# Kernel tuning notes

Hardware: AMD Instinct MI355X
Metric: run time of the kernel (lower is better)

The kernel has to match this reference:

```python
import jax, jax.numpy as jnp
import numpy as np

B, C_IN, C_OUT, T, K, STRIDE, PAD = 16, 256, 256, 4096, 3, 1, 1


def deform_conv1d(x, offset, weight, bias):
    # x: (B,C,T); offset: (B,2K,Tout,1) interleaved (dy,dx); weight: (O,C,K); bias: (O,)
    Bn, C, Tn = x.shape
    O, _, Kn = weight.shape
    dy = offset[:, 0::2, :, 0]  # (B,K,Tout)
    dx = offset[:, 1::2, :, 0]  # (B,K,Tout)
    Tout = dy.shape[-1]
    # offset_mode='center': subtract dcn_base_offset (y base = k-pad, x base = 0)
    base_y = jnp.arange(Kn, dtype=x.dtype) - PAD
    dy = dy - base_y[None, :, None]
    # sampling position along T: t*stride - pad + k + dy
    t0 = jnp.arange(Tout, dtype=x.dtype) * STRIDE - PAD
    py = t0[None, None, :] + jnp.arange(Kn, dtype=x.dtype)[None, :, None] + dy  # (B,K,Tout)
    i0 = jnp.floor(py)
    frac = py - i0
    i0i = i0.astype(jnp.int32)

    def gather(idx):
        valid = ((idx >= 0) & (idx < Tn)).astype(x.dtype)  # zero padding outside
        idxc = jnp.clip(idx, 0, Tn - 1).reshape(Bn, 1, Kn * Tout)
        v = jnp.take_along_axis(x, jnp.broadcast_to(idxc, (Bn, C, Kn * Tout)), axis=2)
        return v.reshape(Bn, C, Kn, Tout) * valid[:, None]

    # linear interp along T
    v = gather(i0i) * (1.0 - frac)[:, None] + gather(i0i + 1) * frac[:, None]  # (B,C,K,Tout)
    # bilinear weight along the dummy width dim (W=1, base x index 0)
    wx = jnp.maximum(0.0, 1.0 - jnp.abs(dx))  # (B,K,Tout)
    v = v * wx[:, None]
    out = jnp.einsum('bckt,ock->bot', v, weight) + bias[None, :, None]
    return out


def setup_inputs() -> dict:
    key = jax.random.key(0)
    k1, k2, k3, k4 = jax.random.split(key, 4)
    x = jax.random.normal(k1, (B, C_IN, T), dtype=jnp.float32)
    offset = jax.random.normal(k2, (B, 2 * K, T, 1), dtype=jnp.float32)
    fan_in = C_IN * K
    bound = 1.0 / np.sqrt(fan_in)
    weight = jax.random.uniform(k3, (C_OUT, C_IN, K), minval=-bound, maxval=bound, dtype=jnp.float32)
    bias = jax.random.uniform(k4, (C_OUT,), minval=-bound, maxval=bound, dtype=jnp.float32)
    return {"x": x, "offset": offset, "weight": weight, "bias": bias}


def reference(x, offset, weight, bias):
    return deform_conv1d(x, offset, weight, bias)
```

## Files before the change

kernel.cpp:

```cpp
#include <hip/hip_runtime.h>
#include <hip/hip_bf16.h>

typedef __attribute__((ext_vector_type(8))) short bf16x8;
typedef __attribute__((ext_vector_type(4))) float f32x4;

constexpr int NB = 16, CIN = 256, COUT = 256, TDIM = 4096, KS = 3, PADV = 1;
constexpr int TT = 64;
constexpr int NSTEP = 12;

typedef __attribute__((address_space(1))) const unsigned int gu32;
typedef __attribute__((address_space(3))) unsigned int lu32;

static __device__ __forceinline__ ushort f2bf(float f) {
    union { __hip_bfloat16 h; ushort u; } cv;
    cv.h = __float2bfloat16(f);
    return cv.u;
}
static __device__ __forceinline__ float bf2f(ushort u) {
    union { unsigned int u32; float f; } cv;
    cv.u32 = ((unsigned int)u) << 16;
    return cv.f;
}

__global__ __launch_bounds__(256) void prepack_w2(const float* __restrict__ w,
                                                  __hip_bfloat16* __restrict__ wp2) {
    int idx = blockIdx.x * 256 + threadIdx.x;
    if (idx >= NSTEP * COUT * 64) return;
    int e    = idx & 7;
    int lane = (idx >> 3) & 63;
    int mf   = (idx >> 9) & 1;
    int kb   = (idx >> 10) & 1;
    int wid  = (idx >> 11) & 3;
    int ot   = (idx >> 13) & 1;
    int s    = idx >> 14;
    int o = ot * 128 + wid * 32 + mf * 16 + (lane & 15);
    int k = s % 3;
    int c = (s / 3) * 64 + kb * 32 + (lane >> 4) * 8 + e;
    wp2[idx] = __float2bfloat16(w[(o * CIN + c) * KS + k]);
}

__global__ __launch_bounds__(256) void prepack_w(const float* __restrict__ w,
                                                 __hip_bfloat16* __restrict__ wp) {
    int idx = blockIdx.x * 256 + threadIdx.x;
    if (idx >= NSTEP * COUT * 64) return;
    int e  = idx & 7;
    int j  = (idx >> 3) & 7;
    int o  = (idx >> 6) & (COUT - 1);
    int s  = idx >> 14;
    int k  = s % 3;
    int c  = (s / 3) * 64 + ((j ^ (o & 7)) << 3) + e;
    wp[idx] = __float2bfloat16(w[(o * CIN + c) * KS + k]);
}

__global__ __launch_bounds__(256) void transpose_x(const float* __restrict__ x,
                                                   ushort* __restrict__ xT) {
    __shared__ ushort tile[64][72];
    const int b  = blockIdx.z;
    const int c0 = blockIdx.y * 64;
    const int t0 = blockIdx.x * 64;
    const int tid = threadIdx.x;
    {
        const int c  = tid >> 2;
        const int tq = (tid & 3) << 4;
        const float* src = x + ((size_t)(b * CIN + c0 + c)) * TDIM + t0 + tq;
        #pragma unroll
        for (int i = 0; i < 4; ++i) {
            float4 f = *(const float4*)(src + 4 * i);
            tile[tq + 4 * i + 0][c] = f2bf(f.x);
            tile[tq + 4 * i + 1][c] = f2bf(f.y);
            tile[tq + 4 * i + 2][c] = f2bf(f.z);
            tile[tq + 4 * i + 3][c] = f2bf(f.w);
        }
    }
    __syncthreads();
    {
        const int t = tid >> 2;
        const int q = tid & 3;
        const uint4* lp = (const uint4*)&tile[t][q * 16];
        uint4 v0 = lp[0], v1 = lp[1];
        uint4* dst = (uint4*)(xT + ((size_t)b * TDIM + t0 + t) * CIN + c0 + q * 16);
        dst[0] = v0;
        dst[1] = v1;
    }
}

__global__ __launch_bounds__(256, 4) void deform_mfma_xt(
    const ushort* __restrict__ xT,
    const float* __restrict__ off,
    const ushort* __restrict__ wp2,
    const float* __restrict__ bias,
    float* __restrict__ out)
{
    __shared__ ushort v_s[TT * 64];
    __shared__ int4   sP[KS][TT];

    const int tid = threadIdx.x;

    const int bid = blockIdx.x;
    const int q   = bid & 7;
    const int r   = bid >> 3;
    const int b   = 2 * q + (r >> 7);
    const int r2  = r & 127;
    const int ot  = r2 >> 6;
    const int tt0 = (r2 & 63) * TT;

    if (tid < KS * TT) {
        int k = tid >> 6, j = tid & (TT - 1);
        int t = tt0 + j;
        float dyr = off[((b * 2 * KS + 2 * k) * TDIM) + t];
        float dxr = off[((b * 2 * KS + 2 * k + 1) * TDIM) + t];
        float dyk = dyr - (float)(k - PADV);
        float py  = (float)(t - PADV + k) + dyk;
        float i0f = floorf(py);
        float fr  = py - i0f;
        int i0 = (int)i0f, i1 = i0 + 1;
        float wx = fmaxf(0.0f, 1.0f - fabsf(dxr));
        float w0 = (1.0f - fr) * wx * ((i0 >= 0 && i0 < TDIM) ? 1.0f : 0.0f);
        float w1 = fr * wx * ((i1 >= 0 && i1 < TDIM) ? 1.0f : 0.0f);
        int base = min(max(i0, 0), TDIM - 2);
        bool iA = (i0 == base);
        float wa = iA ? w0 : ((i0 + 1 == base) ? w1 : 0.0f);
        float wb = iA ? w1 : ((i0 == base + 1) ? w0 : 0.0f);
        int4 p;
        p.x = base;
        p.y = __float_as_int(wa);
        p.z = __float_as_int(wb);
        p.w = 0;
        sP[k][j] = p;
    }

    const int wid  = tid >> 6;
    const int lane = tid & 63;
    const int lr   = lane & 15;
    const int lg   = lane >> 4;

    const int tg   = tid >> 3;
    const int slot = tid & 7;
    const int t0l  = tg;
    const int t1l  = tg + 32;
    const int voffA = (t0l * 128 + slot * 16) ^ ((t0l & 7) << 4);
    const int voffB = (t1l * 128 + slot * 16) ^ ((t1l & 7) << 4);

    f32x4 acc[2][4];
    #pragma unroll
    for (int i = 0; i < 2; ++i)
        #pragma unroll
        for (int j = 0; j < 4; ++j) acc[i][j] = (f32x4)0.0f;

    const ushort* xTb = xT + (size_t)b * TDIM * CIN;

    __syncthreads();

    bf16x8 af0, af1, af2, af3;
    bf16x8 pk0, pk1;
    {
        const ushort* wslot = wp2 + (size_t)(((0 * 2 + ot) * 4 + wid) * 4) * 512 + lane * 8;
        af0 = *(const bf16x8*)(wslot);
        af1 = *(const bf16x8*)(wslot + 512);
        af2 = *(const bf16x8*)(wslot + 1024);
        af3 = *(const bf16x8*)(wslot + 1536);
        int4 e0 = sP[0][t0l];
        int4 e1 = sP[0][t1l];
        const ushort* rowA = xTb + (size_t)e0.x * CIN + slot * 8;
        const ushort* rowB = xTb + (size_t)e1.x * CIN + slot * 8;
        bf16x8 a0 = *(const bf16x8*)rowA;
        bf16x8 a1 = *(const bf16x8*)(rowA + CIN);
        bf16x8 b0 = *(const bf16x8*)rowB;
        bf16x8 b1 = *(const bf16x8*)(rowB + CIN);
        float wa0 = __int_as_float(e0.y), wb0 = __int_as_float(e0.z);
        float wa1 = __int_as_float(e1.y), wb1 = __int_as_float(e1.z);
        #pragma unroll
        for (int i = 0; i < 8; ++i) {
            pk0[i] = (short)f2bf(bf2f((ushort)a0[i]) * wa0 + bf2f((ushort)a1[i]) * wb0);
            pk1[i] = (short)f2bf(bf2f((ushort)b0[i]) * wa1 + bf2f((ushort)b1[i]) * wb1);
        }
    }

    #pragma unroll 1
    for (int s = 0; s < NSTEP; ++s) {
        const int sn  = (s + 1 < NSTEP) ? s + 1 : NSTEP - 1;
        const int kn  = sn % 3;
        const int cbn = (sn / 3) * 64;

        __builtin_amdgcn_s_barrier();
        __builtin_amdgcn_sched_barrier(0);

        *(bf16x8*)((char*)v_s + voffA) = pk0;
        *(bf16x8*)((char*)v_s + voffB) = pk1;

        const ushort* wslot = wp2 + (size_t)(((sn * 2 + ot) * 4 + wid) * 4) * 512 + lane * 8;
        bf16x8 an0 = *(const bf16x8*)(wslot);
        bf16x8 an1 = *(const bf16x8*)(wslot + 512);
        bf16x8 an2 = *(const bf16x8*)(wslot + 1024);
        bf16x8 an3 = *(const bf16x8*)(wslot + 1536);

        int4 e0 = sP[kn][t0l];
        int4 e1 = sP[kn][t1l];
        const ushort* rowA = xTb + (size_t)e0.x * CIN + cbn + slot * 8;
        const ushort* rowB = xTb + (size_t)e1.x * CIN + cbn + slot * 8;
        bf16x8 ga0 = *(const bf16x8*)rowA;
        bf16x8 ga1 = *(const bf16x8*)(rowA + CIN);
        bf16x8 gb0 = *(const bf16x8*)rowB;
        bf16x8 gb1 = *(const bf16x8*)(rowB + CIN);

        __builtin_amdgcn_sched_barrier(0);
        asm volatile("s_waitcnt lgkmcnt(0)" ::: "memory");
        __builtin_amdgcn_sched_barrier(0);
        __builtin_amdgcn_s_barrier();
        __builtin_amdgcn_sched_barrier(0);

        #pragma unroll
        for (int kb = 0; kb < 2; ++kb) {
            const int kk = kb * 32 + lg * 8;
            bf16x8 bfr[4];
            #pragma unroll
            for (int nf = 0; nf < 4; ++nf) {
                int tc = nf * 16 + lr;
                int byte = (tc * 128 + kk * 2) ^ ((tc & 7) << 4);
                bfr[nf] = *(const bf16x8*)((const char*)v_s + byte);
            }
            bf16x8 a0 = kb ? af2 : af0;
            bf16x8 a1 = kb ? af3 : af1;
            #pragma unroll
            for (int nf = 0; nf < 4; ++nf) {
                acc[0][nf] = __builtin_amdgcn_mfma_f32_16x16x32_bf16(a0, bfr[nf], acc[0][nf], 0, 0, 0);
                acc[1][nf] = __builtin_amdgcn_mfma_f32_16x16x32_bf16(a1, bfr[nf], acc[1][nf], 0, 0, 0);
            }
        }
        __builtin_amdgcn_sched_barrier(0);

        {
            float wa0 = __int_as_float(e0.y), wb0 = __int_as_float(e0.z);
            float wa1 = __int_as_float(e1.y), wb1 = __int_as_float(e1.z);
            #pragma unroll
            for (int i = 0; i < 8; ++i) {
                pk0[i] = (short)f2bf(bf2f((ushort)ga0[i]) * wa0 + bf2f((ushort)ga1[i]) * wb0);
                pk1[i] = (short)f2bf(bf2f((ushort)gb0[i]) * wa1 + bf2f((ushort)gb1[i]) * wb1);
            }
        }
        af0 = an0; af1 = an1; af2 = an2; af3 = an3;
    }

    #pragma unroll
    for (int mf = 0; mf < 2; ++mf) {
        #pragma unroll
        for (int rg = 0; rg < 4; ++rg) {
            int o = ot * 128 + wid * 32 + mf * 16 + lg * 4 + rg;
            float bv = bias[o];
            float* orow = out + (size_t)(b * COUT + o) * TDIM + tt0;
            #pragma unroll
            for (int nf = 0; nf < 4; ++nf)
                orow[nf * 16 + lr] = acc[mf][nf][rg] + bv;
        }
    }
}

__global__ __launch_bounds__(512, 4) void deform_mfma_gather(
    const float* __restrict__ x,
    const float* __restrict__ off,
    const __hip_bfloat16* __restrict__ wp,
    const float* __restrict__ bias,
    float* __restrict__ out)
{
    __shared__ ushort w_s[COUT * 64];
    __shared__ ushort v_s[128 * 64];
    __shared__ int4   sP[KS][128];

    const int tid = threadIdx.x;
    const int bid  = blockIdx.x;
    const int q    = bid & 7;
    const int r    = bid >> 3;
    const int b    = 2 * q + (r >> 5);
    const int tt0  = (r & 31) * 128;

    if (tid < KS * 128) {
        int k = tid >> 7, j = tid & 127;
        int t = tt0 + j;
        float dyr = off[((b * 2 * KS + 2 * k) * TDIM) + t];
        float dxr = off[((b * 2 * KS + 2 * k + 1) * TDIM) + t];
        float py  = (float)(t - PADV + k) + dyr - (float)(k - PADV);
        float i0f = floorf(py);
        float fr  = py - i0f;
        int i0 = (int)i0f, i1 = i0 + 1;
        float wx = fmaxf(0.0f, 1.0f - fabsf(dxr));
        float w0 = (1.0f - fr) * wx * ((i0 >= 0 && i0 < TDIM) ? 1.0f : 0.0f);
        float w1 = fr * wx * ((i1 >= 0 && i1 < TDIM) ? 1.0f : 0.0f);
        int4 p;
        p.x = min(max(i0, 0), TDIM - 1);
        p.y = min(max(i1, 0), TDIM - 1);
        p.z = __float_as_int(w0);
        p.w = __float_as_int(w1);
        sP[k][j] = p;
    }

    const int wid    = tid >> 6;
    const int lane   = tid & 63;
    const int o_base = (wid >> 1) * 64;
    const int t_base = (wid & 1) * 64;
    const int lr     = lane & 15;
    const int lg     = lane >> 4;

    f32x4 acc[4][4];
    #pragma unroll
    for (int i = 0; i < 4; ++i)
        #pragma unroll
        for (int j = 0; j < 4; ++j) acc[i][j] = (f32x4)0.0f;

    const float* xb = x + (size_t)b * CIN * TDIM;

    for (int cb = 0; cb < 4; ++cb) {
      for (int k = 0; k < 3; ++k) {
        const int s_idx = cb * 3 + k;
        const int c0    = cb * 64;
        __syncthreads();
        {
            const char* gbase = (const char*)wp + (size_t)s_idx * 32768 + wid * 4096 + lane * 16;
            char* lbase = (char*)w_s + wid * 4096;
            #pragma unroll
            for (int i = 0; i < 4; ++i)
                __builtin_amdgcn_global_load_lds((gu32*)(gbase + i * 1024),
                                                 (lu32*)(lbase + i * 1024), 16, 0, 0);
        }
        {
            const int coct0 = tid >> 7;
            const int t     = tid & 127;
            int4 p = sP[k][t];
            const float* xr0 = xb + (size_t)(c0 + coct0 * 8) * TDIM;
            const float* xr1 = xr0 + (size_t)32 * TDIM;
            float g0[16], g1[16];
            #pragma unroll
            for (int i = 0; i < 8; ++i) {
                g0[2 * i]     = xr0[p.x];
                g0[2 * i + 1] = xr0[p.y];
                xr0 += TDIM;
            }
            #pragma unroll
            for (int i = 0; i < 8; ++i) {
                g1[2 * i]     = xr1[p.x];
                g1[2 * i + 1] = xr1[p.y];
                xr1 += TDIM;
            }
            float w0 = __int_as_float(p.z), w1 = __int_as_float(p.w);
            bf16x8 pk0, pk1;
            #pragma unroll
            for (int i = 0; i < 8; ++i) {
                pk0[i] = (short)f2bf(g0[2 * i] * w0 + g0[2 * i + 1] * w1);
                pk1[i] = (short)f2bf(g1[2 * i] * w0 + g1[2 * i + 1] * w1);
            }
            int row = t * 128;
            int swz = (t & 7) << 4;
            *(bf16x8*)((char*)v_s + ((row + coct0 * 16) ^ swz))       = pk0;
            *(bf16x8*)((char*)v_s + ((row + (coct0 + 4) * 16) ^ swz)) = pk1;
        }
        __syncthreads();
        #pragma unroll
        for (int kb = 0; kb < 2; ++kb) {
            const int kk = kb * 32 + lg * 8;
            bf16x8 bfr[4];
            #pragma unroll
            for (int nf = 0; nf < 4; ++nf) {
                int tc = t_base + nf * 16 + lr;
                int byte = (tc * 128 + kk * 2) ^ ((tc & 7) << 4);
                bfr[nf] = *(const bf16x8*)((const char*)v_s + byte);
            }
            #pragma unroll
            for (int mf = 0; mf < 4; ++mf) {
                int o  = o_base + mf * 16 + lr;
                int byte = (o * 128 + kk * 2) ^ ((o & 7) << 4);
                bf16x8 af = *(const bf16x8*)((const char*)w_s + byte);
                #pragma unroll
                for (int nf = 0; nf < 4; ++nf)
                    acc[mf][nf] = __builtin_amdgcn_mfma_f32_16x16x32_bf16(
                        af, bfr[nf], acc[mf][nf], 0, 0, 0);
            }
        }
      }
    }

    #pragma unroll
    for (int mf = 0; mf < 4; ++mf) {
        #pragma unroll
        for (int rg = 0; rg < 4; ++rg) {
            int o = o_base + mf * 16 + lg * 4 + rg;
            float bv = bias[o];
            float* orow = out + (size_t)(b * COUT + o) * TDIM + tt0 + t_base;
            #pragma unroll
            for (int nf = 0; nf < 4; ++nf)
                orow[nf * 16 + lr] = acc[mf][nf][rg] + bv;
        }
    }
}

extern "C" void kernel_launch(void* const* d_in, const int* in_sizes, int n_in,
                              void* d_out, int out_size, void* d_ws, size_t ws_size,
                              hipStream_t stream) {
    const float* x    = (const float*)d_in[0];
    const float* off  = (const float*)d_in[1];
    const float* w    = (const float*)d_in[2];
    const float* bias = (const float*)d_in[3];
    float* out = (float*)d_out;

    const size_t xt_off  = 512 * 1024;
    const size_t xt_need = xt_off + (size_t)NB * TDIM * CIN * sizeof(ushort);

    if (ws_size >= xt_need) {
        ushort* wp2 = (ushort*)d_ws;
        ushort* xT  = (ushort*)((char*)d_ws + xt_off);
        prepack_w2<<<dim3(768), dim3(256), 0, stream>>>(w, (__hip_bfloat16*)wp2);
        transpose_x<<<dim3(TDIM / 64, CIN / 64, NB), dim3(256), 0, stream>>>(x, xT);
        deform_mfma_xt<<<dim3(2048), dim3(256), 0, stream>>>(xT, off, wp2, bias, out);
    } else {
        __hip_bfloat16* wp = (__hip_bfloat16*)d_ws;
        prepack_w<<<dim3(768), dim3(256), 0, stream>>>(w, wp);
        deform_mfma_gather<<<dim3(512), dim3(512), 0, stream>>>(x, off, wp, bias, out);
    }
}
```

Measured before the change: 70.86 us.

## Fuse weight prepack into transpose, use packed bf16 interpolation and nontemporal stores

Merges the weight prepack kernel into the x transpose kernel, removing one launch. The interpolation now runs as packed bf16x2 multiply-adds with weights pre-rounded to bf16 and duplicated into both halves, where it previously unpacked to float. Row offsets are pre-multiplied by CIN, and output stores are marked nontemporal. The bf16 arithmetic lowers interpolation precision, which risks a larger numeric error.

```diff
diff --git a/kernel.cpp b/kernel.cpp
--- a/kernel.cpp
+++ b/kernel.cpp
@@ -3,6 +3,7 @@
 
 typedef __attribute__((ext_vector_type(8))) short bf16x8;
 typedef __attribute__((ext_vector_type(4))) float f32x4;
+typedef __attribute__((ext_vector_type(2))) __bf16 bf16x2v;
 
 constexpr int NB = 16, CIN = 256, COUT = 256, TDIM = 4096, KS = 3, PADV = 1;
 constexpr int TT = 64;
@@ -16,27 +17,72 @@
     cv.h = __float2bfloat16(f);
     return cv.u;
 }
-static __device__ __forceinline__ float bf2f(ushort u) {
-    union { unsigned int u32; float f; } cv;
-    cv.u32 = ((unsigned int)u) << 16;
-    return cv.f;
-}
-
-__global__ __launch_bounds__(256) void prepack_w2(const float* __restrict__ w,
-                                                  __hip_bfloat16* __restrict__ wp2) {
-    int idx = blockIdx.x * 256 + threadIdx.x;
-    if (idx >= NSTEP * COUT * 64) return;
-    int e    = idx & 7;
-    int lane = (idx >> 3) & 63;
-    int mf   = (idx >> 9) & 1;
-    int kb   = (idx >> 10) & 1;
-    int wid  = (idx >> 11) & 3;
-    int ot   = (idx >> 13) & 1;
-    int s    = idx >> 14;
-    int o = ot * 128 + wid * 32 + mf * 16 + (lane & 15);
-    int k = s % 3;
-    int c = (s / 3) * 64 + kb * 32 + (lane >> 4) * 8 + e;
-    wp2[idx] = __float2bfloat16(w[(o * CIN + c) * KS + k]);
+
+static __device__ __forceinline__ bf16x8 interp8_pk(bf16x8 a0, bf16x8 a1,
+                                                    unsigned int waa, unsigned int wbb) {
+    union U { unsigned int u; bf16x2v v; };
+    union { bf16x8 v; unsigned int u[4]; } A0, A1, R;
+    A0.v = a0; A1.v = a1;
+    U wa2; wa2.u = waa;
+    U wb2; wb2.u = wbb;
+    #pragma unroll
+    for (int j = 0; j < 4; ++j) {
+        U p0; p0.u = A0.u[j];
+        U p1; p1.u = A1.u[j];
+        U r;  r.v = p0.v * wa2.v + p1.v * wb2.v;
+        R.u[j] = r.u;
+    }
+    return R.v;
+}
+
+__global__ __launch_bounds__(256) void transpose_prepack(
+    const float* __restrict__ x, ushort* __restrict__ xT,
+    const float* __restrict__ w, __hip_bfloat16* __restrict__ wp2) {
+    __shared__ ushort tile[64][72];
+    const int b  = blockIdx.z;
+    const int c0 = blockIdx.y * 64;
+    const int t0 = blockIdx.x * 64;
+    const int tid = threadIdx.x;
+    {
+        int gid = ((blockIdx.z * gridDim.y + blockIdx.y) * gridDim.x + blockIdx.x);
+        if (tid < 48) {
+            int idx = gid * 48 + tid;
+            int e    = idx & 7;
+            int lane = (idx >> 3) & 63;
+            int mf   = (idx >> 9) & 1;
+            int kb   = (idx >> 10) & 1;
+            int wid  = (idx >> 11) & 3;
+            int ot   = (idx >> 13) & 1;
+            int s    = idx >> 14;
+            int o = ot * 128 + wid * 32 + mf * 16 + (lane & 15);
+            int k = s % 3;
+            int c = (s / 3) * 64 + kb * 32 + (lane >> 4) * 8 + e;
+            wp2[idx] = __float2bfloat16(w[(o * CIN + c) * KS + k]);
+        }
+    }
+    {
+        const int c  = tid >> 2;
+        const int tq = (tid & 3) << 4;
+        const float* src = x + ((size_t)(b * CIN + c0 + c)) * TDIM + t0 + tq;
+        #pragma unroll
+        for (int i = 0; i < 4; ++i) {
+            float4 f = *(const float4*)(src + 4 * i);
+            tile[tq + 4 * i + 0][c] = f2bf(f.x);
+            tile[tq + 4 * i + 1][c] = f2bf(f.y);
+            tile[tq + 4 * i + 2][c] = f2bf(f.z);
+            tile[tq + 4 * i + 3][c] = f2bf(f.w);
+        }
+    }
+    __syncthreads();
+    {
+        const int t = tid >> 2;
+        const int q = tid & 3;
+        const uint4* lp = (const uint4*)&tile[t][q * 16];
+        uint4 v0 = lp[0], v1 = lp[1];
+        uint4* dst = (uint4*)(xT + ((size_t)b * TDIM + t0 + t) * CIN + c0 + q * 16);
+        dst[0] = v0;
+        dst[1] = v1;
+    }
 }
 
 __global__ __launch_bounds__(256) void prepack_w(const float* __restrict__ w,
@@ -50,38 +96,6 @@
     int k  = s % 3;
     int c  = (s / 3) * 64 + ((j ^ (o & 7)) << 3) + e;
     wp[idx] = __float2bfloat16(w[(o * CIN + c) * KS + k]);
-}
-
-__global__ __launch_bounds__(256) void transpose_x(const float* __restrict__ x,
-                                                   ushort* __restrict__ xT) {
-    __shared__ ushort tile[64][72];
-    const int b  = blockIdx.z;
-    const int c0 = blockIdx.y * 64;
-    const int t0 = blockIdx.x * 64;
-    const int tid = threadIdx.x;
-    {
-        const int c  = tid >> 2;
-        const int tq = (tid & 3) << 4;
-        const float* src = x + ((size_t)(b * CIN + c0 + c)) * TDIM + t0 + tq;
-        #pragma unroll
-        for (int i = 0; i < 4; ++i) {
-            float4 f = *(const float4*)(src + 4 * i);
-            tile[tq + 4 * i + 0][c] = f2bf(f.x);
-            tile[tq + 4 * i + 1][c] = f2bf(f.y);
-            tile[tq + 4 * i + 2][c] = f2bf(f.z);
-            tile[tq + 4 * i + 3][c] = f2bf(f.w);
-        }
-    }
-    __syncthreads();
-    {
-        const int t = tid >> 2;
-        const int q = tid & 3;
-        const uint4* lp = (const uint4*)&tile[t][q * 16];
-        uint4 v0 = lp[0], v1 = lp[1];
-        uint4* dst = (uint4*)(xT + ((size_t)b * TDIM + t0 + t) * CIN + c0 + q * 16);
-        dst[0] = v0;
-        dst[1] = v1;
-    }
 }
 
 __global__ __launch_bounds__(256, 4) void deform_mfma_xt(
@@ -121,10 +135,12 @@
         bool iA = (i0 == base);
         float wa = iA ? w0 : ((i0 + 1 == base) ? w1 : 0.0f);
         float wb = iA ? w1 : ((i0 == base + 1) ? w0 : 0.0f);
+        unsigned int wau = (unsigned)f2bf(wa);
+        unsigned int wbu = (unsigned)f2bf(wb);
         int4 p;
-        p.x = base;
-        p.y = __float_as_int(wa);
-        p.z = __float_as_int(wb);
+        p.x = base * CIN;
+        p.y = (int)(wau | (wau << 16));
+        p.z = (int)(wbu | (wbu << 16));
         p.w = 0;
         sP[k][j] = p;
     }
@@ -161,19 +177,14 @@
         af3 = *(const bf16x8*)(wslot + 1536);
         int4 e0 = sP[0][t0l];
         int4 e1 = sP[0][t1l];
-        const ushort* rowA = xTb + (size_t)e0.x * CIN + slot * 8;
-        const ushort* rowB = xTb + (size_t)e1.x * CIN + slot * 8;
+        const ushort* rowA = xTb + e0.x + slot * 8;
+        const ushort* rowB = xTb + e1.x + slot * 8;
         bf16x8 a0 = *(const bf16x8*)rowA;
         bf16x8 a1 = *(const bf16x8*)(rowA + CIN);
         bf16x8 b0 = *(const bf16x8*)rowB;
         bf16x8 b1 = *(const bf16x8*)(rowB + CIN);
-        float wa0 = __int_as_float(e0.y), wb0 = __int_as_float(e0.z);
-        float wa1 = __int_as_float(e1.y), wb1 = __int_as_float(e1.z);
-        #pragma unroll
-        for (int i = 0; i < 8; ++i) {
-            pk0[i] = (short)f2bf(bf2f((ushort)a0[i]) * wa0 + bf2f((ushort)a1[i]) * wb0);
-            pk1[i] = (short)f2bf(bf2f((ushort)b0[i]) * wa1 + bf2f((ushort)b1[i]) * wb1);
-        }
+        pk0 = interp8_pk(a0, a1, (unsigned)e0.y, (unsigned)e0.z);
+        pk1 = interp8_pk(b0, b1, (unsigned)e1.y, (unsigned)e1.z);
     }
 
     #pragma unroll 1
@@ -196,8 +207,8 @@
 
         int4 e0 = sP[kn][t0l];
         int4 e1 = sP[kn][t1l];
-        const ushort* rowA = xTb + (size_t)e0.x * CIN + cbn + slot * 8;
-        const ushort* rowB = xTb + (size_t)e1.x * CIN + cbn + slot * 8;
+        const ushort* rowA = xTb + e0.x + cbn + slot * 8;
+        const ushort* rowB = xTb + e1.x + cbn + slot * 8;
         bf16x8 ga0 = *(const bf16x8*)rowA;
         bf16x8 ga1 = *(const bf16x8*)(rowA + CIN);
         bf16x8 gb0 = *(const bf16x8*)rowB;
@@ -229,15 +240,8 @@
         }
         __builtin_amdgcn_sched_barrier(0);
 
-        {
-            float wa0 = __int_as_float(e0.y), wb0 = __int_as_float(e0.z);
-            float wa1 = __int_as_float(e1.y), wb1 = __int_as_float(e1.z);
-            #pragma unroll
-            for (int i = 0; i < 8; ++i) {
-                pk0[i] = (short)f2bf(bf2f((ushort)ga0[i]) * wa0 + bf2f((ushort)ga1[i]) * wb0);
-                pk1[i] = (short)f2bf(bf2f((ushort)gb0[i]) * wa1 + bf2f((ushort)gb1[i]) * wb1);
-            }
-        }
+        pk0 = interp8_pk(ga0, ga1, (unsigned)e0.y, (unsigned)e0.z);
+        pk1 = interp8_pk(gb0, gb1, (unsigned)e1.y, (unsigned)e1.z);
         af0 = an0; af1 = an1; af2 = an2; af3 = an3;
     }
 
@@ -250,7 +254,7 @@
             float* orow = out + (size_t)(b * COUT + o) * TDIM + tt0;
             #pragma unroll
             for (int nf = 0; nf < 4; ++nf)
-                orow[nf * 16 + lr] = acc[mf][nf][rg] + bv;
+                __builtin_nontemporal_store(acc[mf][nf][rg] + bv, &orow[nf * 16 + lr]);
         }
     }
 }
@@ -406,8 +410,8 @@
     if (ws_size >= xt_need) {
         ushort* wp2 = (ushort*)d_ws;
         ushort* xT  = (ushort*)((char*)d_ws + xt_off);
-        prepack_w2<<<dim3(768), dim3(256), 0, stream>>>(w, (__hip_bfloat16*)wp2);
-        transpose_x<<<dim3(TDIM / 64, CIN / 64, NB), dim3(256), 0, stream>>>(x, xT);
+        transpose_prepack<<<dim3(TDIM / 64, CIN / 64, NB), dim3(256), 0, stream>>>(
+            x, xT, w, (__hip_bfloat16*)wp2);
         deform_mfma_xt<<<dim3(2048), dim3(256), 0, stream>>>(xT, off, wp2, bias, out);
     } else {
         __hip_bfloat16* wp = (__hip_bfloat16*)d_ws;
```

Result: faster. 69.30 us (-2.2%).
